# Kernel tuning notes

Hardware: AMD Instinct MI355X
Metric: run time of the kernel (lower is better)

Reference implementation:

```python
import jax, jax.numpy as jnp
import numpy as np
import math

D, H, FF = 1024, 16, 4096
B, L = 4, 1024

def setup_inputs() -> dict:
    key = jax.random.key(0)
    ks = jax.random.split(key, 20)
    g = lambda k, shp: jax.random.normal(k, shp, dtype=jnp.float32) * 0.02
    inp = {
        'x': jax.random.normal(ks[0], (B, L, D), dtype=jnp.float32),
        'encoder_output': jax.random.normal(ks[1], (B, L, D), dtype=jnp.float32),
        'src_mask': jnp.ones((1, 1, L, L), dtype=jnp.int32),
        'tgt_mask': jnp.tril(jnp.ones((L, L), dtype=jnp.int32))[None, None],
        'wq': g(ks[2], (D, D)), 'bq': jnp.zeros((D,), jnp.float32),
        'wk': g(ks[3], (D, D)), 'bk': jnp.zeros((D,), jnp.float32),
        'wv': g(ks[4], (D, D)), 'bv': jnp.zeros((D,), jnp.float32),
        'wo': g(ks[5], (D, D)), 'bo': jnp.zeros((D,), jnp.float32),
        'w1': g(ks[6], (FF, D)), 'b1': jnp.zeros((FF,), jnp.float32),
        'w2': g(ks[7], (D, FF)), 'b2': jnp.zeros((D,), jnp.float32),
        'g1': jnp.ones((D,), jnp.float32), 'be1': jnp.zeros((D,), jnp.float32),
        'g2': jnp.ones((D,), jnp.float32), 'be2': jnp.zeros((D,), jnp.float32),
    }
    return inp

def _layernorm(x, g, b, eps=1e-5):
    mu = jnp.mean(x, axis=-1, keepdims=True)
    var = jnp.var(x, axis=-1, keepdims=True)
    return (x - mu) * jax.lax.rsqrt(var + eps) * g + b

def _mha(q, k, v, mask, wq, bq, wk, bk, wv, bv, wo, bo):
    Bq, Lq, C = q.shape
    dh = C // H
    qh = (q @ wq.T + bq).reshape(Bq, Lq, H, dh)      # b q h d
    kh = (k @ wk.T + bk).reshape(Bq, -1, H, dh)       # b k h d
    vh = (v @ wv.T + bv).reshape(Bq, -1, H, dh)
    # NOTE: source scales by sqrt(C) (full model dim), not sqrt(head_dim)
    scores = jnp.einsum('bqhd,bkhd->bhqk', qh, kh) / math.sqrt(C)
    if mask is not None:
        scores = jnp.where(mask == 0, jnp.float32(-1e9), scores)
    attn = jax.nn.softmax(scores, axis=-1)
    out = jnp.einsum('bhqk,bkhd->bqhd', attn, vh).reshape(Bq, Lq, C)
    return out @ wo.T + bo

def reference(x, encoder_output, src_mask, tgt_mask,
              wq, bq, wk, bk, wv, bv, wo, bo,
              w1, b1, w2, b2, g1, be1, g2, be2):
    # self-attention (dropout identity in eval mode)
    y1 = _mha(x, x, x, tgt_mask, wq, bq, wk, bk, wv, bv, wo, bo)
    y1 = _layernorm(y1 + x, g1, be1)
    # cross-attention: source reuses attn1 weights and layer_norm1 (faithful)
    y2 = _mha(y1, encoder_output, encoder_output, src_mask, wq, bq, wk, bk, wv, bv, wo, bo)
    y2 = _layernorm(y1 + y2, g1, be1)
    # FFN + layer_norm2
    y = jax.nn.relu(y2 @ w1.T + b1) @ w2.T + b2
    return _layernorm(y2 + y, g2, be2)
```

## Files before the change

### kernel.cpp

```cpp
#include <hip/hip_runtime.h>
#include <hip/hip_bf16.h>

typedef __attribute__((ext_vector_type(8))) short short8;
typedef __attribute__((ext_vector_type(4))) float f32x4;
typedef __attribute__((ext_vector_type(4))) unsigned short ushort4v;

#define MFMA_BF16(a, b, c) __builtin_amdgcn_mfma_f32_16x16x32_bf16((a), (b), (c), 0, 0, 0)
#define AS1 __attribute__((address_space(1)))
#define AS3 __attribute__((address_space(3)))

__device__ __forceinline__ unsigned short f2b(float f) {
  unsigned u = __float_as_uint(f);
  u += 0x7fffu + ((u >> 16) & 1u);
  return (unsigned short)(u >> 16);
}

__device__ __forceinline__ size_t kpack_idx(int row, int col) {
  int b = row >> 10, l = row & 1023, h = col >> 6, d = col & 63;
  return ((size_t)(b * 16 + h) << 16) + l * 64 + (d ^ ((l & 7) << 3));
}

__global__ __launch_bounds__(256) void cast8(
    const float* s0, const float* s1, const float* s2, const float* s3,
    const float* s4, const float* s5, const float* s6, const float* s7,
    unsigned short* d0, unsigned short* d1, unsigned short* d2, unsigned short* d3,
    unsigned short* d4, unsigned short* d5, unsigned short* d6, unsigned short* d7,
    int n0, int n1, int n2, int n3, int n4, int n5, int n6, int n7) {
  const float* s; unsigned short* d; int n;
  switch (blockIdx.y) {
    case 0: s = s0; d = d0; n = n0; break;
    case 1: s = s1; d = d1; n = n1; break;
    case 2: s = s2; d = d2; n = n2; break;
    case 3: s = s3; d = d3; n = n3; break;
    case 4: s = s4; d = d4; n = n4; break;
    case 5: s = s5; d = d5; n = n5; break;
    case 6: s = s6; d = d6; n = n6; break;
    default: s = s7; d = d7; n = n7; break;
  }
  int stride = gridDim.x * blockDim.x;
  for (int i = blockIdx.x * blockDim.x + threadIdx.x; i < n; i += stride) {
    float4 v = reinterpret_cast<const float4*>(s)[i];
    ushort4v o;
    o.x = f2b(v.x); o.y = f2b(v.y); o.z = f2b(v.z); o.w = f2b(v.w);
    reinterpret_cast<ushort4v*>(d)[i] = o;
  }
}

template <int RELU, int RES, int OUTF, int OUTB, int TM>
__global__ __launch_bounds__(256) void gemm_bt(
    const unsigned short* __restrict__ A, const unsigned short* __restrict__ W,
    const float* __restrict__ bias, const float* __restrict__ resid,
    float* __restrict__ outF, unsigned short* __restrict__ outB,
    int M, int N, int K) {
  constexpr int MI = TM / 32;
  __shared__ unsigned short lA[TM * 64];
  __shared__ unsigned short lB[128 * 64];
  int nbn = N >> 7;
  int nwg = gridDim.x;
  int id = blockIdx.x;
  { int q = nwg >> 3; id = (id & 7) * q + (id >> 3); }
  int m0 = (id / nbn) * TM, n0 = (id % nbn) << 7;
  int lane = threadIdx.x & 63, wave = threadIdx.x >> 6;
  int wr = (wave >> 1) * (TM / 2), wc = (wave & 1) * 64;
  int rq = lane & 15, kq = (lane >> 4) * 8;
  int xr8 = (rq & 7) << 3;
  f32x4 acc[MI][4] = {};

  int t8 = threadIdx.x * 8;
  for (int kt = 0; kt < K; kt += 64) {
#pragma unroll
    for (int i = 0; i < MI; ++i) {
      int e = t8 + i * 2048;
      int row = e >> 6;
      int gcol = (((e >> 3) & 7) ^ (row & 7)) << 3;
      __builtin_amdgcn_global_load_lds(
          (const AS1 void*)(A + (size_t)(m0 + row) * K + kt + gcol),
          (AS3 void*)(lA + e), 16, 0, 0);
    }
#pragma unroll
    for (int i = 0; i < 4; ++i) {
      int e = t8 + i * 2048;
      int row = e >> 6;
      int gcol = (((e >> 3) & 7) ^ (row & 7)) << 3;
      __builtin_amdgcn_global_load_lds(
          (const AS1 void*)(W + (size_t)(n0 + row) * K + kt + gcol),
          (AS3 void*)(lB + e), 16, 0, 0);
    }
    __syncthreads();
#pragma unroll
    for (int s = 0; s < 2; ++s) {
      short8 af[MI], bf[4];
#pragma unroll
      for (int i = 0; i < MI; ++i)
        af[i] = *reinterpret_cast<const short8*>(lA + (wr + i * 16 + rq) * 64 + ((s * 32 + kq) ^ xr8));
#pragma unroll
      for (int j = 0; j < 4; ++j)
        bf[j] = *reinterpret_cast<const short8*>(lB + (wc + j * 16 + rq) * 64 + ((s * 32 + kq) ^ xr8));
#pragma unroll
      for (int i = 0; i < MI; ++i)
#pragma unroll
        for (int j = 0; j < 4; ++j)
          acc[i][j] = MFMA_BF16(af[i], bf[j], acc[i][j]);
    }
    __syncthreads();
  }

  int r0 = (lane >> 4) * 4;
#pragma unroll
  for (int i = 0; i < MI; ++i) {
#pragma unroll
    for (int j = 0; j < 4; ++j) {
      int row = m0 + wr + i * 16 + r0;
      int col = n0 + wc + j * 16 + rq;
      float bv = bias[col];
#pragma unroll
      for (int r = 0; r < 4; ++r) {
        float v = acc[i][j][r] + bv;
        if (RES) v += resid[(size_t)(row + r) * N + col];
        if (RELU) v = fmaxf(v, 0.0f);
        if (OUTF) outF[(size_t)(row + r) * N + col] = v;
        if (OUTB) outB[(size_t)(row + r) * N + col] = f2b(v);
      }
    }
  }
}

__global__ __launch_bounds__(256, 4) void gemm_qkv(
    const unsigned short* __restrict__ xb, const unsigned short* __restrict__ encb,
    const unsigned short* __restrict__ wq, const unsigned short* __restrict__ wk,
    const unsigned short* __restrict__ wv,
    const float* __restrict__ bq, const float* __restrict__ bk, const float* __restrict__ bv,
    unsigned short* __restrict__ qb, unsigned short* __restrict__ kp1,
    unsigned short* __restrict__ vp1, unsigned short* __restrict__ kp2,
    unsigned short* __restrict__ vp2) {
  __shared__ unsigned short lA[2][128 * 32];
  __shared__ unsigned short lB[2][128 * 32];
  int id = blockIdx.x;
  id = (id & 7) * 160 + (id >> 3);
  int im = id / 40, jn = id % 40;
  int sel = jn >> 3;
  int m0 = im << 7, col0 = (jn & 7) << 7;
  const unsigned short* A = (sel < 3) ? xb : encb;
  const unsigned short* Wm = (sel == 0) ? wq : ((sel == 1 || sel == 3) ? wk : wv);
  const float* bias = (sel == 0) ? bq : ((sel == 1 || sel == 3) ? bk : bv);
  int lane = threadIdx.x & 63, wave = threadIdx.x >> 6;
  int wr = (wave >> 1) * 64, wc = (wave & 1) * 64;
  int rq = lane & 15, kq = (lane >> 4) * 8;
  f32x4 acc[4][4] = {};

  int e0 = threadIdx.x * 8;
#define STAGE_QKV(KT, BUF)                                                      \
  {                                                                             \
    _Pragma("unroll") for (int i = 0; i < 2; ++i) {                             \
      int e = e0 + i * 2048;                                                    \
      int row = e >> 5, col = e & 31;                                           \
      __builtin_amdgcn_global_load_lds(                                         \
          (const AS1 void*)(A + (size_t)(m0 + row) * 1024 + (KT) + col),        \
          (AS3 void*)(&lA[BUF][e]), 16, 0, 0);                                  \
      __builtin_amdgcn_global_load_lds(                                         \
          (const AS1 void*)(Wm + (size_t)(col0 + row) * 1024 + (KT) + col),     \
          (AS3 void*)(&lB[BUF][e]), 16, 0, 0);                                  \
    }                                                                           \
  }

  STAGE_QKV(0, 0);
  __syncthreads();
  for (int t = 0; t < 32; ++t) {
    int cur = t & 1;
    if (t + 1 < 32) STAGE_QKV((t + 1) << 5, cur ^ 1);
    short8 af[4], bf[4];
#pragma unroll
    for (int i = 0; i < 4; ++i)
      af[i] = *reinterpret_cast<const short8*>(&lA[cur][(wr + i * 16 + rq) * 32 + kq]);
#pragma unroll
    for (int j = 0; j < 4; ++j)
      bf[j] = *reinterpret_cast<const short8*>(&lB[cur][(wc + j * 16 + rq) * 32 + kq]);
#pragma unroll
    for (int i = 0; i < 4; ++i)
#pragma unroll
      for (int j = 0; j < 4; ++j)
        acc[i][j] = MFMA_BF16(af[i], bf[j], acc[i][j]);
    __syncthreads();
  }
#undef STAGE_QKV

  unsigned short* outp = (sel == 0) ? qb : (sel == 1) ? kp1 : (sel == 2) ? vp1
                         : (sel == 3) ? kp2 : vp2;
  int pack = (sel == 0) ? 0 : ((sel == 1 || sel == 3) ? 1 : 2);
  int r0 = (lane >> 4) * 4;
#pragma unroll
  for (int i = 0; i < 4; ++i) {
#pragma unroll
    for (int j = 0; j < 4; ++j) {
      int row0 = m0 + wr + i * 16 + r0;
      int col = col0 + wc + j * 16 + rq;
      float bv = bias[col];
      if (pack == 2) {
        int b = row0 >> 10, k0 = row0 & 1023, h = col >> 6, d = col & 63;
        size_t idx = ((size_t)((b * 16 + h) * 16 + (k0 >> 6)) << 12) + d * 64 + ((k0 & 63) ^ ((d & 7) << 3));
        ushort4v o;
        o.x = f2b(acc[i][j][0] + bv);
        o.y = f2b(acc[i][j][1] + bv);
        o.z = f2b(acc[i][j][2] + bv);
        o.w = f2b(acc[i][j][3] + bv);
        *reinterpret_cast<ushort4v*>(&outp[idx]) = o;
      } else {
#pragma unroll
        for (int r = 0; r < 4; ++r) {
          int row = row0 + r;
          float v = acc[i][j][r] + bv;
          if (pack == 0) outp[(size_t)row * 1024 + col] = f2b(v);
          else outp[kpack_idx(row, col)] = f2b(v);
        }
      }
    }
  }
}

__device__ __forceinline__ void attn_step(
    const unsigned short* __restrict__ kcur, const unsigned short* __restrict__ vcur,
    unsigned short* __restrict__ plw, const short8* qf,
    f32x4* accd, float& m2, float& lsum,
    int rq, int hi, int kq, int xr, int wave, bool domask) {
  const float SC = 0.04508422f;
  f32x4 st[4];
  __builtin_amdgcn_s_setprio(1);
#pragma unroll
  for (int sub = 0; sub < 4; ++sub) {
    f32x4 z = {0.f, 0.f, 0.f, 0.f};
#pragma unroll
    for (int c = 0; c < 2; ++c) {
      short8 kf = *reinterpret_cast<const short8*>(
          &kcur[(sub * 16 + rq) * 64 + ((c * 32 + hi * 8) ^ xr)]);
      z = MFMA_BF16(kf, qf[c], z);
    }
    st[sub] = z * SC;
  }
  __builtin_amdgcn_s_setprio(0);
  if (domask) {
#pragma unroll
    for (int sub = 0; sub < 4; ++sub)
#pragma unroll
      for (int r = 0; r < 4; ++r)
        if (sub * 16 + hi * 4 + r > wave * 16 + rq) st[sub][r] = -1e9f;
  }
  f32x4 t0 = {fmaxf(st[0][0], st[1][0]), fmaxf(st[0][1], st[1][1]),
              fmaxf(st[0][2], st[1][2]), fmaxf(st[0][3], st[1][3])};
  f32x4 t1 = {fmaxf(st[2][0], st[3][0]), fmaxf(st[2][1], st[3][1]),
              fmaxf(st[2][2], st[3][2]), fmaxf(st[2][3], st[3][3])};
  float mx = fmaxf(fmaxf(fmaxf(t0[0], t1[0]), fmaxf(t0[1], t1[1])),
                   fmaxf(fmaxf(t0[2], t1[2]), fmaxf(t0[3], t1[3])));
  mx = fmaxf(mx, __shfl_xor(mx, 16, 64));
  mx = fmaxf(mx, __shfl_xor(mx, 32, 64));
  float mn = fmaxf(m2, mx);
  float al = exp2f(m2 - mn);
  m2 = mn;
  f32x4 e[4];
#pragma unroll
  for (int sub = 0; sub < 4; ++sub)
#pragma unroll
    for (int r = 0; r < 4; ++r) e[sub][r] = exp2f(st[sub][r] - mn);
  f32x4 s01 = e[0] + e[1], s23 = e[2] + e[3];
  f32x4 s = s01 + s23;
  float ps = (s[0] + s[1]) + (s[2] + s[3]);
  ps += __shfl_xor(ps, 16, 64);
  ps += __shfl_xor(ps, 32, 64);
  lsum = lsum * al + ps;
#pragma unroll
  for (int sub = 0; sub < 4; ++sub) {
    unsigned w0 = (unsigned)f2b(e[sub][0]) | ((unsigned)f2b(e[sub][1]) << 16);
    unsigned w1 = (unsigned)f2b(e[sub][2]) | ((unsigned)f2b(e[sub][3]) << 16);
    uint2 w = make_uint2(w0, w1);
    *reinterpret_cast<uint2*>(&plw[rq * 64 + ((sub * 16 + hi * 4) ^ xr)]) = w;
  }
  float alb[4];
#pragma unroll
  for (int r = 0; r < 4; ++r) alb[r] = __shfl(al, hi * 4 + r, 64);
#pragma unroll
  for (int d = 0; d < 4; ++d)
#pragma unroll
    for (int r = 0; r < 4; ++r) accd[d][r] *= alb[r];
  short8 pf[2];
#pragma unroll
  for (int c = 0; c < 2; ++c)
    pf[c] = *reinterpret_cast<const short8*>(&plw[rq * 64 + ((c * 32 + hi * 8) ^ xr)]);
  __builtin_amdgcn_s_setprio(1);
#pragma unroll
  for (int d = 0; d < 4; ++d) {
#pragma unroll
    for (int c = 0; c < 2; ++c) {
      short8 vf = *reinterpret_cast<const short8*>(
          &vcur[(d * 16 + rq) * 64 + ((c * 32 + hi * 8) ^ xr)]);
      accd[d] = MFMA_BF16(pf[c], vf, accd[d]);
    }
  }
  __builtin_amdgcn_s_setprio(0);
}

__global__ __launch_bounds__(256) void attn_kernel(
    const unsigned short* __restrict__ Q, const unsigned short* __restrict__ Kp,
    const unsigned short* __restrict__ Vp, unsigned short* __restrict__ O, int causal) {
  __shared__ unsigned short kls[2][4096];
  __shared__ unsigned short vls[2][4096];
  __shared__ unsigned short pls[4][1024];
  int id = blockIdx.x;
  int xcd = id & 7, j = id >> 3;
  int bh = xcd * 8 + (j & 7);
  int b = bh >> 4, h = bh & 15;
  int lane = threadIdx.x & 63, wave = threadIdx.x >> 6;
  int rq = lane & 15, hi = lane >> 4, kq = hi * 8;
  int xr = (rq & 7) << 3;
  int sb = wave * 1024 + lane * 8;
  const unsigned short* Kbh = Kp + ((size_t)bh << 16);
  const unsigned short* Vbh = Vp + ((size_t)bh << 16);
  unsigned short* plw = pls[wave];

  int p = j >> 3;
  int qtA = p;
  int qtB = causal ? (15 - p) : (p + 8);
  int lastA = causal ? qtA : 15;
  int nkt = causal ? (qtB + 1) : 16;

  int qrowA = qtA * 64 + wave * 16, qrowB = qtB * 64 + wave * 16;
  short8 qfA[2], qfB[2];
#pragma unroll
  for (int c = 0; c < 2; ++c) {
    qfA[c] = *reinterpret_cast<const short8*>(
        Q + (size_t)(b * 1024 + qrowA + rq) * 1024 + h * 64 + c * 32 + kq);
    qfB[c] = *reinterpret_cast<const short8*>(
        Q + (size_t)(b * 1024 + qrowB + rq) * 1024 + h * 64 + c * 32 + kq);
  }

  float mA = -1e30f, lsA = 0.f, mB = -1e30f, lsB = 0.f;
  f32x4 accA[4] = {}, accB[4] = {};

#pragma unroll
  for (int i = 0; i < 2; ++i) {
    __builtin_amdgcn_global_load_lds((const AS1 void*)(Kbh + sb + i * 512),
                                     (AS3 void*)(&kls[0][sb + i * 512]), 16, 0, 0);
    __builtin_amdgcn_global_load_lds((const AS1 void*)(Vbh + sb + i * 512),
                                     (AS3 void*)(&vls[0][sb + i * 512]), 16, 0, 0);
  }
  __syncthreads();

  int cur = 0;
  for (int kt = 0; kt < nkt; ++kt) {
    if (kt + 1 < nkt) {
      const unsigned short* kg = Kbh + (kt + 1) * 4096 + sb;
      const unsigned short* vg = Vbh + (kt + 1) * 4096 + sb;
#pragma unroll
      for (int i = 0; i < 2; ++i) {
        __builtin_amdgcn_global_load_lds((const AS1 void*)(kg + i * 512),
                                         (AS3 void*)(&kls[cur ^ 1][sb + i * 512]), 16, 0, 0);
        __builtin_amdgcn_global_load_lds((const AS1 void*)(vg + i * 512),
                                         (AS3 void*)(&vls[cur ^ 1][sb + i * 512]), 16, 0, 0);
      }
    }
    attn_step(kls[cur], vls[cur], plw, qfB, accB, mB, lsB, rq, hi, kq, xr, wave,
              causal && kt == qtB);
    if (kt <= lastA)
      attn_step(kls[cur], vls[cur], plw, qfA, accA, mA, lsA, rq, hi, kq, xr, wave,
                causal && kt == qtA);
    __syncthreads();
    cur ^= 1;
  }

  float lbA[4], lbB[4];
#pragma unroll
  for (int r = 0; r < 4; ++r) {
    lbA[r] = 1.0f / __shfl(lsA, hi * 4 + r, 64);
    lbB[r] = 1.0f / __shfl(lsB, hi * 4 + r, 64);
  }
#pragma unroll
  for (int d = 0; d < 4; ++d)
#pragma unroll
    for (int r = 0; r < 4; ++r) {
      O[(size_t)(b * 1024 + qrowA + hi * 4 + r) * 1024 + h * 64 + d * 16 + rq] =
          f2b(accA[d][r] * lbA[r]);
      O[(size_t)(b * 1024 + qrowB + hi * 4 + r) * 1024 + h * 64 + d * 16 + rq] =
          f2b(accB[d][r] * lbB[r]);
    }
}

template <int OUTF, int OUTB>
__global__ __launch_bounds__(256) void ln_kernel(const float* __restrict__ X,
                                                 const float* __restrict__ g,
                                                 const float* __restrict__ be,
                                                 float* __restrict__ outF,
                                                 unsigned short* __restrict__ outB) {
  __shared__ float red[2][4];
  int row = blockIdx.x;
  int t = threadIdx.x;
  const float* xr = X + (size_t)row * 1024;
  float4 v = reinterpret_cast<const float4*>(xr)[t];
  float s = v.x + v.y + v.z + v.w;
  float ss = v.x * v.x + v.y * v.y + v.z * v.z + v.w * v.w;
#pragma unroll
  for (int off = 1; off < 64; off <<= 1) {
    s += __shfl_xor(s, off, 64);
    ss += __shfl_xor(ss, off, 64);
  }
  int wave = t >> 6;
  if ((t & 63) == 0) { red[0][wave] = s; red[1][wave] = ss; }
  __syncthreads();
  s = red[0][0] + red[0][1] + red[0][2] + red[0][3];
  ss = red[1][0] + red[1][1] + red[1][2] + red[1][3];
  float mu = s * (1.f / 1024.f);
  float var = ss * (1.f / 1024.f) - mu * mu;
  float rs = rsqrtf(var + 1e-5f);
  float4 gv = reinterpret_cast<const float4*>(g)[t];
  float4 bv = reinterpret_cast<const float4*>(be)[t];
  float o0 = (v.x - mu) * rs * gv.x + bv.x;
  float o1 = (v.y - mu) * rs * gv.y + bv.y;
  float o2 = (v.z - mu) * rs * gv.z + bv.z;
  float o3 = (v.w - mu) * rs * gv.w + bv.w;
  if (OUTF) {
    float4 o = make_float4(o0, o1, o2, o3);
    reinterpret_cast<float4*>(outF + (size_t)row * 1024)[t] = o;
  }
  if (OUTB) {
    ushort4v o;
    o.x = f2b(o0); o.y = f2b(o1); o.z = f2b(o2); o.w = f2b(o3);
    reinterpret_cast<ushort4v*>(outB + (size_t)row * 1024)[t] = o;
  }
}

extern "C" void kernel_launch(void* const* d_in, const int* in_sizes, int n_in,
                              void* d_out, int out_size, void* d_ws, size_t ws_size,
                              hipStream_t stream) {
  const float* x   = (const float*)d_in[0];
  const float* enc = (const float*)d_in[1];
  const float* wq = (const float*)d_in[4];  const float* bq = (const float*)d_in[5];
  const float* wk = (const float*)d_in[6];  const float* bk = (const float*)d_in[7];
  const float* wv = (const float*)d_in[8];  const float* bv = (const float*)d_in[9];
  const float* wo = (const float*)d_in[10]; const float* bo = (const float*)d_in[11];
  const float* w1 = (const float*)d_in[12]; const float* b1 = (const float*)d_in[13];
  const float* w2 = (const float*)d_in[14]; const float* b2 = (const float*)d_in[15];
  const float* g1 = (const float*)d_in[16]; const float* be1 = (const float*)d_in[17];
  const float* g2 = (const float*)d_in[18]; const float* be2 = (const float*)d_in[19];
  float* out = (float*)d_out;

  const int M = 4096;
  char* ws = (char*)d_ws;
  size_t off = 0;
  auto alloc = [&](size_t bytes) -> char* {
    char* p = ws + off;
    off += (bytes + 255) & ~(size_t)255;
    return p;
  };
  unsigned short* xb   = (unsigned short*)alloc((size_t)M * 1024 * 2);
  unsigned short* encb = (unsigned short*)alloc((size_t)M * 1024 * 2);
  unsigned short* wqb  = (unsigned short*)alloc((size_t)1024 * 1024 * 2);
  unsigned short* wkb  = (unsigned short*)alloc((size_t)1024 * 1024 * 2);
  unsigned short* wvb  = (unsigned short*)alloc((size_t)1024 * 1024 * 2);
  unsigned short* wob  = (unsigned short*)alloc((size_t)1024 * 1024 * 2);
  unsigned short* w1b  = (unsigned short*)alloc((size_t)4096 * 1024 * 2);
  unsigned short* w2b  = (unsigned short*)alloc((size_t)4096 * 1024 * 2);
  unsigned short* qb   = (unsigned short*)alloc((size_t)M * 1024 * 2);
  unsigned short* kp1  = (unsigned short*)alloc((size_t)M * 1024 * 2);
  unsigned short* vp1  = (unsigned short*)alloc((size_t)M * 1024 * 2);
  unsigned short* kp2  = (unsigned short*)alloc((size_t)M * 1024 * 2);
  unsigned short* vp2  = (unsigned short*)alloc((size_t)M * 1024 * 2);
  unsigned short* ab   = (unsigned short*)alloc((size_t)M * 1024 * 2);
  float* s1 = (float*)alloc((size_t)M * 1024 * 4);
  float* y1 = (float*)alloc((size_t)M * 1024 * 4);
  unsigned short* hb = kp1;
  unsigned short* y1b = xb;
  unsigned short* y2b = qb;
  float* y2 = y1;

  dim3 b256(256);
  cast8<<<dim3(256, 8), b256, 0, stream>>>(
      x, enc, wq, wk, wv, wo, w1, w2,
      xb, encb, wqb, wkb, wvb, wob, w1b, w2b,
      M * 1024 / 4, M * 1024 / 4, 262144, 262144, 262144, 262144,
      4096 * 1024 / 4, 4096 * 1024 / 4);

  gemm_qkv<<<1280, b256, 0, stream>>>(xb, encb, wqb, wkb, wvb, bq, bk, bv,
                                      qb, kp1, vp1, kp2, vp2);

  attn_kernel<<<512, b256, 0, stream>>>(qb, kp1, vp1, ab, 1);
  gemm_bt<0, 1, 1, 0, 64><<<512, b256, 0, stream>>>(ab, wob, bo, x, s1, nullptr, M, 1024, 1024);
  ln_kernel<1, 1><<<4096, b256, 0, stream>>>(s1, g1, be1, y1, y1b);

  gemm_bt<0, 0, 0, 1, 64><<<512, b256, 0, stream>>>(y1b, wqb, bq, nullptr, nullptr, qb, M, 1024, 1024);
  attn_kernel<<<512, b256, 0, stream>>>(qb, kp2, vp2, ab, 0);
  gemm_bt<0, 1, 1, 0, 64><<<512, b256, 0, stream>>>(ab, wob, bo, y1, s1, nullptr, M, 1024, 1024);
  ln_kernel<1, 1><<<4096, b256, 0, stream>>>(s1, g1, be1, y2, y2b);

  gemm_bt<1, 0, 0, 1, 128><<<1024, b256, 0, stream>>>(y2b, w1b, b1, nullptr, nullptr, hb, M, 4096, 1024);
  gemm_bt<0, 1, 1, 0, 64><<<512, b256, 0, stream>>>(hb, w2b, b2, y2, s1, nullptr, M, 1024, 4096);
  ln_kernel<1, 0><<<4096, b256, 0, stream>>>(s1, g2, be2, out, nullptr);

  (void)in_sizes; (void)n_in; (void)out_size; (void)ws_size;
}
```

Baseline: 350.5 us.

## Fuse Q/K/V projections per block to reuse staged A tiles

Each QKV block now computes two or three weight projections (Q,K,V for x; K,V for encoder output) against a single staged A tile, so the A operand is loaded from global memory once instead of once per projection. The grid shrinks from 1280 to 512 blocks and each block holds three sets of accumulators, so launch bounds are lowered to 2 waves per SIMD. The cost is higher register and LDS use, lower occupancy, and load imbalance between blocks that do three projections and blocks that do two.

```diff
diff --git a/kernel.cpp b/kernel.cpp
--- a/kernel.cpp
+++ b/kernel.cpp
@@ -125,7 +125,7 @@
   }
 }
 
-__global__ __launch_bounds__(256, 4) void gemm_qkv(
+__global__ __launch_bounds__(256, 2) void gemm_qkv_f(
     const unsigned short* __restrict__ xb, const unsigned short* __restrict__ encb,
     const unsigned short* __restrict__ wq, const unsigned short* __restrict__ wk,
     const unsigned short* __restrict__ wv,
@@ -133,23 +133,25 @@
     unsigned short* __restrict__ qb, unsigned short* __restrict__ kp1,
     unsigned short* __restrict__ vp1, unsigned short* __restrict__ kp2,
     unsigned short* __restrict__ vp2) {
-  __shared__ unsigned short lA[2][128 * 32];
-  __shared__ unsigned short lB[2][128 * 32];
+  __shared__ unsigned short lA[2][4096];
+  __shared__ unsigned short lB[2][3][4096];
   int id = blockIdx.x;
-  id = (id & 7) * 160 + (id >> 3);
-  int im = id / 40, jn = id % 40;
-  int sel = jn >> 3;
-  int m0 = im << 7, col0 = (jn & 7) << 7;
-  const unsigned short* A = (sel < 3) ? xb : encb;
-  const unsigned short* Wm = (sel == 0) ? wq : ((sel == 1 || sel == 3) ? wk : wv);
-  const float* bias = (sel == 0) ? bq : ((sel == 1 || sel == 3) ? bk : bv);
+  id = (id & 7) * 64 + (id >> 3);
+  int sel = id >> 8;
+  int idx = id & 255;
+  int m0 = (idx >> 3) << 7, col0 = (idx & 7) << 7;
+  int nW = sel ? 2 : 3;
+  const unsigned short* A = sel ? encb : xb;
+  const unsigned short* W0 = sel ? wk : wq;
+  const unsigned short* W1 = sel ? wv : wk;
+  const unsigned short* W2 = wv;
   int lane = threadIdx.x & 63, wave = threadIdx.x >> 6;
   int wr = (wave >> 1) * 64, wc = (wave & 1) * 64;
   int rq = lane & 15, kq = (lane >> 4) * 8;
-  f32x4 acc[4][4] = {};
+  f32x4 acc[3][4][4] = {};
 
   int e0 = threadIdx.x * 8;
-#define STAGE_QKV(KT, BUF)                                                      \
+#define STG(KT, BUF)                                                            \
   {                                                                             \
     _Pragma("unroll") for (int i = 0; i < 2; ++i) {                             \
       int e = e0 + i * 2048;                                                    \
@@ -158,59 +160,76 @@
           (const AS1 void*)(A + (size_t)(m0 + row) * 1024 + (KT) + col),        \
           (AS3 void*)(&lA[BUF][e]), 16, 0, 0);                                  \
       __builtin_amdgcn_global_load_lds(                                         \
-          (const AS1 void*)(Wm + (size_t)(col0 + row) * 1024 + (KT) + col),     \
-          (AS3 void*)(&lB[BUF][e]), 16, 0, 0);                                  \
+          (const AS1 void*)(W0 + (size_t)(col0 + row) * 1024 + (KT) + col),     \
+          (AS3 void*)(&lB[BUF][0][e]), 16, 0, 0);                               \
+      __builtin_amdgcn_global_load_lds(                                         \
+          (const AS1 void*)(W1 + (size_t)(col0 + row) * 1024 + (KT) + col),     \
+          (AS3 void*)(&lB[BUF][1][e]), 16, 0, 0);                               \
+      if (!sel)                                                                 \
+        __builtin_amdgcn_global_load_lds(                                       \
+            (const AS1 void*)(W2 + (size_t)(col0 + row) * 1024 + (KT) + col),   \
+            (AS3 void*)(&lB[BUF][2][e]), 16, 0, 0);                             \
     }                                                                           \
   }
 
-  STAGE_QKV(0, 0);
+  STG(0, 0);
   __syncthreads();
   for (int t = 0; t < 32; ++t) {
     int cur = t & 1;
-    if (t + 1 < 32) STAGE_QKV((t + 1) << 5, cur ^ 1);
-    short8 af[4], bf[4];
+    if (t + 1 < 32) STG((t + 1) << 5, cur ^ 1);
+    short8 af[4];
 #pragma unroll
     for (int i = 0; i < 4; ++i)
       af[i] = *reinterpret_cast<const short8*>(&lA[cur][(wr + i * 16 + rq) * 32 + kq]);
 #pragma unroll
-    for (int j = 0; j < 4; ++j)
-      bf[j] = *reinterpret_cast<const short8*>(&lB[cur][(wc + j * 16 + rq) * 32 + kq]);
-#pragma unroll
-    for (int i = 0; i < 4; ++i)
-#pragma unroll
-      for (int j = 0; j < 4; ++j)
-        acc[i][j] = MFMA_BF16(af[i], bf[j], acc[i][j]);
+    for (int w = 0; w < 3; ++w) {
+      if (w < nW) {
+        short8 bf[4];
+#pragma unroll
+        for (int j = 0; j < 4; ++j)
+          bf[j] = *reinterpret_cast<const short8*>(&lB[cur][w][(wc + j * 16 + rq) * 32 + kq]);
+#pragma unroll
+        for (int i = 0; i < 4; ++i)
+#pragma unroll
+          for (int j = 0; j < 4; ++j)
+            acc[w][i][j] = MFMA_BF16(af[i], bf[j], acc[w][i][j]);
+      }
+    }
     __syncthreads();
   }
-#undef STAGE_QKV
-
-  unsigned short* outp = (sel == 0) ? qb : (sel == 1) ? kp1 : (sel == 2) ? vp1
-                         : (sel == 3) ? kp2 : vp2;
-  int pack = (sel == 0) ? 0 : ((sel == 1 || sel == 3) ? 1 : 2);
+#undef STG
+
   int r0 = (lane >> 4) * 4;
 #pragma unroll
-  for (int i = 0; i < 4; ++i) {
-#pragma unroll
-    for (int j = 0; j < 4; ++j) {
-      int row0 = m0 + wr + i * 16 + r0;
-      int col = col0 + wc + j * 16 + rq;
-      float bv = bias[col];
-      if (pack == 2) {
-        int b = row0 >> 10, k0 = row0 & 1023, h = col >> 6, d = col & 63;
-        size_t idx = ((size_t)((b * 16 + h) * 16 + (k0 >> 6)) << 12) + d * 64 + ((k0 & 63) ^ ((d & 7) << 3));
-        ushort4v o;
-        o.x = f2b(acc[i][j][0] + bv);
-        o.y = f2b(acc[i][j][1] + bv);
-        o.z = f2b(acc[i][j][2] + bv);
-        o.w = f2b(acc[i][j][3] + bv);
-        *reinterpret_cast<ushort4v*>(&outp[idx]) = o;
-      } else {
-#pragma unroll
-        for (int r = 0; r < 4; ++r) {
-          int row = row0 + r;
-          float v = acc[i][j][r] + bv;
-          if (pack == 0) outp[(size_t)row * 1024 + col] = f2b(v);
-          else outp[kpack_idx(row, col)] = f2b(v);
+  for (int w = 0; w < 3; ++w) {
+    if (w >= nW) continue;
+    const float* bias = sel ? (w == 0 ? bk : bv) : (w == 0 ? bq : (w == 1 ? bk : bv));
+    unsigned short* outp = sel ? (w == 0 ? kp2 : vp2) : (w == 0 ? qb : (w == 1 ? kp1 : vp1));
+    int pack = sel ? (w + 1) : w;
+#pragma unroll
+    for (int i = 0; i < 4; ++i) {
+#pragma unroll
+      for (int j = 0; j < 4; ++j) {
+        int row0 = m0 + wr + i * 16 + r0;
+        int col = col0 + wc + j * 16 + rq;
+        float bv2 = bias[col];
+        if (pack == 2) {
+          int b = row0 >> 10, k0 = row0 & 1023, h = col >> 6, d = col & 63;
+          size_t idx2 = ((size_t)((b * 16 + h) * 16 + (k0 >> 6)) << 12) + d * 64 + ((k0 & 63) ^ ((d & 7) << 3));
+          ushort4v o;
+          o.x = f2b(acc[w][i][j][0] + bv2);
+          o.y = f2b(acc[w][i][j][1] + bv2);
+          o.z = f2b(acc[w][i][j][2] + bv2);
+          o.w = f2b(acc[w][i][j][3] + bv2);
+          *reinterpret_cast<ushort4v*>(&outp[idx2]) = o;
+        } else {
+#pragma unroll
+          for (int r = 0; r < 4; ++r) {
+            int row = row0 + r;
+            float v = acc[w][i][j][r] + bv2;
+            if (pack == 0) outp[(size_t)row * 1024 + col] = f2b(v);
+            else outp[kpack_idx(row, col)] = f2b(v);
+          }
         }
       }
     }
@@ -476,8 +495,8 @@
       M * 1024 / 4, M * 1024 / 4, 262144, 262144, 262144, 262144,
       4096 * 1024 / 4, 4096 * 1024 / 4);
 
-  gemm_qkv<<<1280, b256, 0, stream>>>(xb, encb, wqb, wkb, wvb, bq, bk, bv,
-                                      qb, kp1, vp1, kp2, vp2);
+  gemm_qkv_f<<<512, b256, 0, stream>>>(xb, encb, wqb, wkb, wvb, bq, bk, bv,
+                                       qb, kp1, vp1, kp2, vp2);
 
   attn_kernel<<<512, b256, 0, stream>>>(qb, kp1, vp1, ab, 1);
   gemm_bt<0, 1, 1, 0, 64><<<512, b256, 0, stream>>>(ab, wob, bo, x, s1, nullptr, M, 1024, 1024);
```

Measured after the change: 341.5 us. 2.6% less time.
